# Performance work log

Hardware: AMD Instinct MI355X
Metric: run time of the kernel (lower is better)

Reference implementation:

```python
import jax, jax.numpy as jnp
import numpy as np

B, S, D, H = 4, 2048, 1024, 16
HD = D // H  # head_dim = 64


def setup_inputs() -> dict:
    key = jax.random.key(0)
    ks = jax.random.split(key, 11)
    scale = 1.0 / np.sqrt(D)
    q = jax.random.normal(ks[0], (B, S, D), jnp.float32)
    k = jax.random.normal(ks[1], (B, S, D), jnp.float32)
    v = jax.random.normal(ks[2], (B, S, D), jnp.float32)
    # causal mask, broadcastable over [B, H, Sq, Sk]
    mask = jnp.tril(jnp.ones((S, S), bool))[None, None, :, :]
    Wq = jax.random.normal(ks[3], (D, D), jnp.float32) * scale
    bq = jnp.zeros((D,), jnp.float32)
    Wk = jax.random.normal(ks[4], (D, D), jnp.float32) * scale
    bk = jnp.zeros((D,), jnp.float32)
    Wv = jax.random.normal(ks[5], (D, D), jnp.float32) * scale
    bv = jnp.zeros((D,), jnp.float32)
    Wo = jax.random.normal(ks[6], (D, D), jnp.float32) * scale
    bo = jnp.zeros((D,), jnp.float32)
    return {"q": q, "k": k, "v": v, "mask": mask,
            "Wq": Wq, "bq": bq, "Wk": Wk, "bk": bk,
            "Wv": Wv, "bv": bv, "Wo": Wo, "bo": bo}


def reference(q, k, v, mask, Wq, bq, Wk, bk, Wv, bv, Wo, bo):
    b, sq, _ = q.shape
    sk = k.shape[1]
    # projections (torch Linear: x @ W.T + b)
    qh = (q @ Wq.T + bq).reshape(b, sq, H, HD)
    kh = (k @ Wk.T + bk).reshape(b, sk, H, HD)
    vh = (v @ Wv.T + bv).reshape(b, sk, H, HD)
    # scaled dot-product attention: [b, h, sq, sk]
    scores = jnp.einsum('bqhd,bkhd->bhqk', qh, kh) / jnp.sqrt(jnp.float32(HD))
    scores = jnp.where(mask, scores, jnp.float32(-jnp.inf))
    attn = jax.nn.softmax(scores, axis=-1)
    out = jnp.einsum('bhqk,bkhd->bqhd', attn, vh).reshape(b, sq, D)
    return out @ Wo.T + bo
```

## Files before the change

### kernel.cpp

```cpp
#include <hip/hip_runtime.h>
#include <hip/hip_bf16.h>
#include <cstdint>
#include <cstddef>

typedef __attribute__((ext_vector_type(4))) float f32x4;
typedef __attribute__((ext_vector_type(8))) __bf16 bf16x8;

constexpr int Bc = 4, Sc = 2048, Dc = 1024, Hc = 16, HDc = 64;
constexpr int Mrows = Bc * Sc;
constexpr int Kdim = Dc;

__device__ __forceinline__ void gload_lds16(const void* g, void* lds) {
  __builtin_amdgcn_global_load_lds(
      (const __attribute__((address_space(1))) void*)g,
      (__attribute__((address_space(3))) void*)lds, 16, 0, 0);
}

__global__ void cvt4_f32_to_bf16(const float* __restrict__ s0, const float* __restrict__ s1,
                                 const float* __restrict__ s2, const float* __restrict__ s3,
                                 __bf16* __restrict__ d0, __bf16* __restrict__ d1,
                                 __bf16* __restrict__ d2, __bf16* __restrict__ d3, int n4each) {
  int i = blockIdx.x * blockDim.x + threadIdx.x;
  int which = i / n4each, j = i - which * n4each;
  const float* s = which == 0 ? s0 : which == 1 ? s1 : which == 2 ? s2 : s3;
  __bf16* d = which == 0 ? d0 : which == 1 ? d1 : which == 2 ? d2 : d3;
  float4 f = ((const float4*)s)[j];
  union { __bf16 h[4]; uint2 u; } p;
  p.h[0] = (__bf16)f.x; p.h[1] = (__bf16)f.y;
  p.h[2] = (__bf16)f.z; p.h[3] = (__bf16)f.w;
  ((uint2*)d)[j] = p.u;
}

__global__ __launch_bounds__(256, 2)
void gemm_qkv(const float* __restrict__ qin, const float* __restrict__ kin,
              const float* __restrict__ vin, const __bf16* __restrict__ Wcat,
              const float* __restrict__ bq, const float* __restrict__ bk,
              const float* __restrict__ bv,
              __bf16* __restrict__ Qh, __bf16* __restrict__ Kh,
              __bf16* __restrict__ Vt, float qscale)
{
  __shared__ __align__(16) __bf16 As[128 * 32];
  __shared__ __align__(16) __bf16 Bs[128 * 32];
  const int tid = threadIdx.x;
  const int wave = tid >> 6, lane = tid & 63;
  const int wr = wave >> 1, wc = wave & 1;
  const int r = lane & 15, hi = lane >> 4;
  const int lin = (int)blockIdx.y * 24 + (int)blockIdx.x;
  const int xcd = lin & 7, s8 = lin >> 3;
  const int my = (xcd << 3) | (s8 / 24);
  const int mx = s8 % 24;
  const int m0 = my * 128, n0 = mx * 128;
  const int proj = n0 >> 10;
  const float* Xa = proj == 0 ? qin : proj == 1 ? kin : vin;

  f32x4 acc[4][4] = {};

  for (int k0 = 0; k0 < Kdim; k0 += 32) {
    #pragma unroll
    for (int c = 0; c < 2; ++c) {
      int chunk = c * 256 + tid;
      int row = chunk >> 2;
      int cw = chunk & 3;
      int hc = cw ^ (row & 3);
      const float* src = Xa + (size_t)(m0 + row) * Kdim + k0 + hc * 8;
      float4 f0 = *(const float4*)src;
      float4 f1 = *(const float4*)(src + 4);
      union { __bf16 h[8]; uint4 u; } pk;
      pk.h[0] = (__bf16)f0.x; pk.h[1] = (__bf16)f0.y;
      pk.h[2] = (__bf16)f0.z; pk.h[3] = (__bf16)f0.w;
      pk.h[4] = (__bf16)f1.x; pk.h[5] = (__bf16)f1.y;
      pk.h[6] = (__bf16)f1.z; pk.h[7] = (__bf16)f1.w;
      *(uint4*)&As[(size_t)chunk * 8] = pk.u;
    }
    #pragma unroll
    for (int c = 0; c < 2; ++c) {
      int chunk = c * 256 + wave * 64 + lane;
      int row = chunk >> 2;
      int hc = (chunk & 3) ^ (row & 3);
      gload_lds16(Wcat + (size_t)(n0 + row) * Kdim + k0 + hc * 8,
                  &Bs[(size_t)(c * 256 + wave * 64) * 8]);
    }
    __syncthreads();
    bf16x8 af[4], bfr[4];
    #pragma unroll
    for (int m = 0; m < 4; ++m) {
      int rowl = wr * 64 + m * 16 + r;
      af[m] = *(const bf16x8*)&As[rowl * 32 + ((hi ^ (rowl & 3)) * 8)];
    }
    #pragma unroll
    for (int n = 0; n < 4; ++n) {
      int rowl = wc * 64 + n * 16 + r;
      bfr[n] = *(const bf16x8*)&Bs[rowl * 32 + ((hi ^ (rowl & 3)) * 8)];
    }
    #pragma unroll
    for (int m = 0; m < 4; ++m)
      #pragma unroll
      for (int n = 0; n < 4; ++n)
        acc[m][n] = __builtin_amdgcn_mfma_f32_16x16x32_bf16(af[m], bfr[n], acc[m][n], 0, 0, 0);
    __syncthreads();
  }

  const float* bias = proj == 0 ? bq : proj == 1 ? bk : bv;
  if (proj < 2) {
    __bf16* out = proj == 0 ? Qh : Kh;
    const float sc = proj == 0 ? qscale : 1.0f;
    #pragma unroll
    for (int m = 0; m < 4; ++m)
      #pragma unroll
      for (int n = 0; n < 4; ++n)
        #pragma unroll
        for (int rg = 0; rg < 4; ++rg) {
          int row_g = m0 + wr * 64 + m * 16 + hi * 4 + rg;
          int col_g = n0 + wc * 64 + n * 16 + r;
          int c = col_g & 1023, h = c >> 6, d = c & 63;
          int b = row_g >> 11, s = row_g & (Sc - 1);
          float v = (acc[m][n][rg] + bias[c]) * sc;
          out[((((size_t)b * Hc + h) * Sc + s) << 6) + d] = (__bf16)v;
        }
  } else {
    #pragma unroll
    for (int m = 0; m < 4; ++m)
      #pragma unroll
      for (int n = 0; n < 4; ++n) {
        int row0 = m0 + wr * 64 + m * 16 + hi * 4;
        int col_g = n0 + wc * 64 + n * 16 + r;
        int c = col_g & 1023, h = c >> 6, d = c & 63;
        int b = row0 >> 11, s = row0 & (Sc - 1);
        union { __bf16 hh[4]; uint2 u; } w;
        #pragma unroll
        for (int rg = 0; rg < 4; ++rg)
          w.hh[rg] = (__bf16)(acc[m][n][rg] + bias[c]);
        *(uint2*)&Vt[((((size_t)b * Hc + h) * HDc + d) << 11) + s] = w.u;
      }
  }
}

__global__ __launch_bounds__(256, 2)
void gemm_out(const __bf16* __restrict__ A, const __bf16* __restrict__ Bw,
              const float* __restrict__ bias, float* __restrict__ outp)
{
  __shared__ __align__(16) __bf16 As[128 * 32];
  __shared__ __align__(16) __bf16 Bs[128 * 32];
  const int tid = threadIdx.x;
  const int wave = tid >> 6, lane = tid & 63;
  const int wr = wave >> 1, wc = wave & 1;
  const int r = lane & 15, hi = lane >> 4;
  const int lin = (int)blockIdx.y * 8 + (int)blockIdx.x;
  const int xcd = lin & 7, s8 = lin >> 3;
  const int m0 = (((xcd << 3) | (s8 >> 3)) ) * 128;
  const int n0 = (s8 & 7) * 128;

  f32x4 acc[4][4] = {};

  for (int k0 = 0; k0 < Kdim; k0 += 32) {
    #pragma unroll
    for (int c = 0; c < 2; ++c) {
      int chunk = c * 256 + wave * 64 + lane;
      int row = chunk >> 2;
      int hc = (chunk & 3) ^ (row & 3);
      gload_lds16(A  + (size_t)(m0 + row) * Kdim + k0 + hc * 8,
                  &As[(size_t)(c * 256 + wave * 64) * 8]);
      gload_lds16(Bw + (size_t)(n0 + row) * Kdim + k0 + hc * 8,
                  &Bs[(size_t)(c * 256 + wave * 64) * 8]);
    }
    __syncthreads();
    bf16x8 af[4], bfr[4];
    #pragma unroll
    for (int m = 0; m < 4; ++m) {
      int rowl = wr * 64 + m * 16 + r;
      af[m] = *(const bf16x8*)&As[rowl * 32 + ((hi ^ (rowl & 3)) * 8)];
    }
    #pragma unroll
    for (int n = 0; n < 4; ++n) {
      int rowl = wc * 64 + n * 16 + r;
      bfr[n] = *(const bf16x8*)&Bs[rowl * 32 + ((hi ^ (rowl & 3)) * 8)];
    }
    #pragma unroll
    for (int m = 0; m < 4; ++m)
      #pragma unroll
      for (int n = 0; n < 4; ++n)
        acc[m][n] = __builtin_amdgcn_mfma_f32_16x16x32_bf16(af[m], bfr[n], acc[m][n], 0, 0, 0);
    __syncthreads();
  }

  #pragma unroll
  for (int m = 0; m < 4; ++m)
    #pragma unroll
    for (int n = 0; n < 4; ++n)
      #pragma unroll
      for (int rg = 0; rg < 4; ++rg) {
        int row_g = m0 + wr * 64 + m * 16 + hi * 4 + rg;
        int col_g = n0 + wc * 64 + n * 16 + r;
        outp[(size_t)row_g * Dc + col_g] = acc[m][n][rg] + bias[col_g];
      }
}

__global__ __launch_bounds__(128, 2)
void attn_causal(const __bf16* __restrict__ Qh, const __bf16* __restrict__ Kh,
                 const __bf16* __restrict__ Vt, __bf16* __restrict__ outp)
{
  __shared__ __align__(16) float OaS[4][4][64][4];
  __shared__ float MS[4][64];
  __shared__ float LS[4][64];

  const int tid = threadIdx.x;
  const int wave = tid >> 6, lane = tid & 63;
  const int r = lane & 15, hi = lane >> 4;
  const int lin = (int)blockIdx.y * 32 + (int)blockIdx.x;
  const int xcd = lin & 7, s8 = lin >> 3;
  const int bh = (xcd << 3) | (s8 >> 5);
  const int qt = 31 - (s8 & 31);
  const int q0 = qt * 64;
  const __bf16* Q = Qh + (size_t)bh * (Sc * HDc);
  const __bf16* K = Kh + (size_t)bh * (Sc * HDc);
  const __bf16* V = Vt + (size_t)bh * (HDc * Sc);

  bf16x8 qf[4][2];
  #pragma unroll
  for (int m = 0; m < 4; ++m)
    #pragma unroll
    for (int kc = 0; kc < 2; ++kc)
      qf[m][kc] = *(const bf16x8*)&Q[(size_t)(q0 + m * 16 + r) * 64 + kc * 32 + hi * 8];

  f32x4 o_acc[4][4] = {};
  float mrow[4], lrow[4];
  #pragma unroll
  for (int m = 0; m < 4; ++m) { mrow[m] = -1e30f; lrow[m] = 0.f; }

  const int T = qt + 1;
  const int half = (T + 1) >> 1;
  const int t0 = wave ? half : 0;
  const int t1 = wave ? T : half;

  bf16x8 kf[4][2], vf[4][2], pb[4][2];

  #pragma unroll
  for (int n = 0; n < 4; ++n)
    #pragma unroll
    for (int kc = 0; kc < 2; ++kc) {
      kf[n][kc] = *(const bf16x8*)&K[(size_t)(t0 * 64 + n * 16 + r) * 64 + kc * 32 + hi * 8];
      vf[n][kc] = *(const bf16x8*)&V[(size_t)(n * 16 + r) * Sc + t0 * 64 + kc * 32 + hi * 8];
    }

  for (int t = t0; t < t1; ++t) {
    const bool diag = (t == T - 1);
    const int kvn = (t + 1) * 64;

    #pragma unroll
    for (int m = 0; m < 4; ++m) {
      f32x4 sn[4];
      __builtin_amdgcn_s_setprio(1);
      #pragma unroll
      for (int n = 0; n < 4; ++n) {
        f32x4 z = {0.f, 0.f, 0.f, 0.f};
        sn[n] = __builtin_amdgcn_mfma_f32_16x16x32_bf16(kf[n][0], qf[m][0], z, 0, 0, 0);
        sn[n] = __builtin_amdgcn_mfma_f32_16x16x32_bf16(kf[n][1], qf[m][1], sn[n], 0, 0, 0);
      }
      __builtin_amdgcn_s_setprio(0);
      if (diag) {
        #pragma unroll
        for (int n = 0; n < 4; ++n)
          #pragma unroll
          for (int rg = 0; rg < 4; ++rg)
            if (n * 16 + hi * 4 + rg > m * 16 + r) sn[n][rg] = -1e30f;
      }
      float mx = fmaxf(fmaxf(fmaxf(sn[0][0], sn[0][1]), fmaxf(sn[0][2], sn[0][3])),
                       fmaxf(fmaxf(sn[1][0], sn[1][1]), fmaxf(sn[1][2], sn[1][3])));
      mx = fmaxf(mx, fmaxf(fmaxf(fmaxf(sn[2][0], sn[2][1]), fmaxf(sn[2][2], sn[2][3])),
                           fmaxf(fmaxf(sn[3][0], sn[3][1]), fmaxf(sn[3][2], sn[3][3]))));
      mx = fmaxf(mx, __shfl_xor(mx, 16));
      mx = fmaxf(mx, __shfl_xor(mx, 32));
      float mloc = mrow[m];
      if (__any(mx > mloc + 8.f)) {
        float mnew = fmaxf(mloc, mx);
        float sc = __builtin_exp2f(mloc - mnew);
        lrow[m] *= sc;
        #pragma unroll
        for (int n = 0; n < 4; ++n) o_acc[m][n] *= sc;
        mrow[m] = mnew; mloc = mnew;
      }
      float rs = 0.f;
      #pragma unroll
      for (int n = 0; n < 4; ++n)
        #pragma unroll
        for (int rg = 0; rg < 4; ++rg) {
          float p = __builtin_exp2f(sn[n][rg] - mloc);
          sn[n][rg] = p;
          rs += p;
        }
      rs += __shfl_xor(rs, 16);
      rs += __shfl_xor(rs, 32);
      lrow[m] += rs;

      #pragma unroll
      for (int kc = 0; kc < 2; ++kc) {
        uint32_t p0a, p0b, p1a, p1b;
        asm("v_cvt_pk_bf16_f32 %0, %1, %2" : "=v"(p0a) : "v"(sn[2*kc][0]),   "v"(sn[2*kc][1]));
        asm("v_cvt_pk_bf16_f32 %0, %1, %2" : "=v"(p0b) : "v"(sn[2*kc][2]),   "v"(sn[2*kc][3]));
        asm("v_cvt_pk_bf16_f32 %0, %1, %2" : "=v"(p1a) : "v"(sn[2*kc+1][0]), "v"(sn[2*kc+1][1]));
        asm("v_cvt_pk_bf16_f32 %0, %1, %2" : "=v"(p1b) : "v"(sn[2*kc+1][2]), "v"(sn[2*kc+1][3]));
        asm("v_permlane32_swap_b32 %0, %1" : "+v"(p0a), "+v"(p1a));
        asm("v_permlane32_swap_b32 %0, %1" : "+v"(p0b), "+v"(p1b));
        uint32_t Xa = (uint32_t)__shfl_xor((int)p1a, 16);
        uint32_t Xb = (uint32_t)__shfl_xor((int)p1b, 16);
        uint32_t Ya = (uint32_t)__shfl_xor((int)p0a, 16);
        uint32_t Yb = (uint32_t)__shfl_xor((int)p0b, 16);
        union { uint32_t u[4]; bf16x8 v; } pk;
        pk.u[0] = (hi & 1) ? Xa : p0a;
        pk.u[1] = (hi & 1) ? Xb : p0b;
        pk.u[2] = (hi & 1) ? p1a : Ya;
        pk.u[3] = (hi & 1) ? p1b : Yb;
        pb[m][kc] = pk.v;
      }
    }

    if (t + 1 < t1) {
      #pragma unroll
      for (int n = 0; n < 4; ++n)
        #pragma unroll
        for (int kc = 0; kc < 2; ++kc)
          kf[n][kc] = *(const bf16x8*)&K[(size_t)(kvn + n * 16 + r) * 64 + kc * 32 + hi * 8];
    }

    __builtin_amdgcn_s_setprio(1);
    #pragma unroll
    for (int m = 0; m < 4; ++m)
      #pragma unroll
      for (int n = 0; n < 4; ++n) {
        o_acc[m][n] = __builtin_amdgcn_mfma_f32_16x16x32_bf16(vf[n][0], pb[m][0], o_acc[m][n], 0, 0, 0);
        o_acc[m][n] = __builtin_amdgcn_mfma_f32_16x16x32_bf16(vf[n][1], pb[m][1], o_acc[m][n], 0, 0, 0);
      }
    __builtin_amdgcn_s_setprio(0);

    if (t + 1 < t1) {
      #pragma unroll
      for (int n = 0; n < 4; ++n)
        #pragma unroll
        for (int kc = 0; kc < 2; ++kc)
          vf[n][kc] = *(const bf16x8*)&V[(size_t)(n * 16 + r) * Sc + kvn + kc * 32 + hi * 8];
    }
  }

  if (wave == 1) {
    #pragma unroll
    for (int m = 0; m < 4; ++m) {
      MS[m][lane] = mrow[m];
      LS[m][lane] = lrow[m];
      #pragma unroll
      for (int n = 0; n < 4; ++n)
        *(f32x4*)OaS[m][n][lane] = o_acc[m][n];
    }
  }
  __syncthreads();
  if (wave == 0) {
    const int b = bh >> 4, h = bh & 15;
    #pragma unroll
    for (int m = 0; m < 4; ++m) {
      float mB = MS[m][lane], lB = LS[m][lane];
      float mF = fmaxf(mrow[m], mB);
      float aA = __builtin_exp2f(mrow[m] - mF);
      float aB = __builtin_exp2f(mB - mF);
      float inv = 1.f / (lrow[m] * aA + lB * aB);
      size_t row = (size_t)b * Sc + q0 + m * 16 + r;
      #pragma unroll
      for (int n = 0; n < 4; ++n) {
        f32x4 oB = *(f32x4*)OaS[m][n][lane];
        union { __bf16 hh[4]; uint2 u; } w;
        #pragma unroll
        for (int rg = 0; rg < 4; ++rg)
          w.hh[rg] = (__bf16)((o_acc[m][n][rg] * aA + oB[rg] * aB) * inv);
        int col = h * 64 + n * 16 + hi * 4;
        *(uint2*)&outp[row * Dc + col] = w.u;
      }
    }
  }
}

extern "C" void kernel_launch(void* const* d_in, const int* in_sizes, int n_in,
                              void* d_out, int out_size, void* d_ws, size_t ws_size,
                              hipStream_t stream) {
  const float* q  = (const float*)d_in[0];
  const float* k  = (const float*)d_in[1];
  const float* v  = (const float*)d_in[2];
  const float* Wq = (const float*)d_in[4];
  const float* bq = (const float*)d_in[5];
  const float* Wk = (const float*)d_in[6];
  const float* bk = (const float*)d_in[7];
  const float* Wv = (const float*)d_in[8];
  const float* bv = (const float*)d_in[9];
  const float* Wo = (const float*)d_in[10];
  const float* bo = (const float*)d_in[11];

  char* ws = (char*)d_ws;
  constexpr size_t MB = 1u << 20;
  __bf16* Wcat = (__bf16*)(ws + 0 * MB);
  __bf16* Wkb  = (__bf16*)(ws + 2 * MB);
  __bf16* Wvb  = (__bf16*)(ws + 4 * MB);
  __bf16* Wob  = (__bf16*)(ws + 6 * MB);
  __bf16* Xbf  = (__bf16*)(ws + 8 * MB);
  __bf16* QhB  = (__bf16*)(ws + 24 * MB);
  __bf16* KhB  = (__bf16*)(ws + 40 * MB);
  __bf16* VtB  = (__bf16*)(ws + 56 * MB);

  const int nW4 = (Dc * Dc) / 4;
  cvt4_f32_to_bf16<<<(4 * nW4) / 256, 256, 0, stream>>>(Wq, Wk, Wv, Wo, Wcat, Wkb, Wvb, Wob, nW4);

  const float qscale = 0.125f * 1.44269504f;
  gemm_qkv<<<dim3(24, Mrows / 128), 256, 0, stream>>>(q, k, v, Wcat, bq, bk, bv,
                                                      QhB, KhB, VtB, qscale);

  attn_causal<<<dim3(32, Bc * Hc), 128, 0, stream>>>(QhB, KhB, VtB, Xbf);

  gemm_out<<<dim3(8, Mrows / 128), 256, 0, stream>>>(Xbf, Wob, bo, (float*)d_out);
}
```

Before: 279.3 us.

## Split causal attention work by paired 32-row query tiles instead of KV halves

Each wave now owns an independent 32-row query tile, pairing a short tile (px) with a long one (63-px) inside a block to balance causal work, instead of two waves splitting one 64-row tile's KV range. This removes the LDS merge of partial softmax states and the block barrier, and halves per-wave accumulator registers. In exchange each wave reloads the full K/V stream for only 32 query rows, so K/V reuse per load is halved, and the diagonal tile still computes a full 64-key block with masking.

```diff
diff --git a/kernel.cpp b/kernel.cpp
--- a/kernel.cpp
+++ b/kernel.cpp
@@ -199,55 +199,50 @@
 void attn_causal(const __bf16* __restrict__ Qh, const __bf16* __restrict__ Kh,
                  const __bf16* __restrict__ Vt, __bf16* __restrict__ outp)
 {
-  __shared__ __align__(16) float OaS[4][4][64][4];
-  __shared__ float MS[4][64];
-  __shared__ float LS[4][64];
-
   const int tid = threadIdx.x;
   const int wave = tid >> 6, lane = tid & 63;
   const int r = lane & 15, hi = lane >> 4;
   const int lin = (int)blockIdx.y * 32 + (int)blockIdx.x;
   const int xcd = lin & 7, s8 = lin >> 3;
   const int bh = (xcd << 3) | (s8 >> 5);
-  const int qt = 31 - (s8 & 31);
-  const int q0 = qt * 64;
+  const int px = s8 & 31;
+  const int qh = wave ? (63 - px) : px;
+  const int q0 = qh * 32;
   const __bf16* Q = Qh + (size_t)bh * (Sc * HDc);
   const __bf16* K = Kh + (size_t)bh * (Sc * HDc);
   const __bf16* V = Vt + (size_t)bh * (HDc * Sc);
 
-  bf16x8 qf[4][2];
-  #pragma unroll
-  for (int m = 0; m < 4; ++m)
+  bf16x8 qf[2][2];
+  #pragma unroll
+  for (int m = 0; m < 2; ++m)
     #pragma unroll
     for (int kc = 0; kc < 2; ++kc)
       qf[m][kc] = *(const bf16x8*)&Q[(size_t)(q0 + m * 16 + r) * 64 + kc * 32 + hi * 8];
 
-  f32x4 o_acc[4][4] = {};
-  float mrow[4], lrow[4];
-  #pragma unroll
-  for (int m = 0; m < 4; ++m) { mrow[m] = -1e30f; lrow[m] = 0.f; }
-
-  const int T = qt + 1;
-  const int half = (T + 1) >> 1;
-  const int t0 = wave ? half : 0;
-  const int t1 = wave ? T : half;
-
-  bf16x8 kf[4][2], vf[4][2], pb[4][2];
+  f32x4 o_acc[2][4] = {};
+  float mrow[2], lrow[2];
+  #pragma unroll
+  for (int m = 0; m < 2; ++m) { mrow[m] = -1e30f; lrow[m] = 0.f; }
+
+  const int T = (qh >> 1) + 1;
+  const int qloc_base = (qh & 1) * 32;
+
+  bf16x8 kf[4][2], vf[4][2], pb[2][2];
 
   #pragma unroll
   for (int n = 0; n < 4; ++n)
     #pragma unroll
     for (int kc = 0; kc < 2; ++kc) {
-      kf[n][kc] = *(const bf16x8*)&K[(size_t)(t0 * 64 + n * 16 + r) * 64 + kc * 32 + hi * 8];
-      vf[n][kc] = *(const bf16x8*)&V[(size_t)(n * 16 + r) * Sc + t0 * 64 + kc * 32 + hi * 8];
-    }
-
-  for (int t = t0; t < t1; ++t) {
+      kf[n][kc] = *(const bf16x8*)&K[(size_t)(n * 16 + r) * 64 + kc * 32 + hi * 8];
+      vf[n][kc] = *(const bf16x8*)&V[(size_t)(n * 16 + r) * Sc + kc * 32 + hi * 8];
+    }
+
+  for (int t = 0; t < T; ++t) {
     const bool diag = (t == T - 1);
     const int kvn = (t + 1) * 64;
 
     #pragma unroll
-    for (int m = 0; m < 4; ++m) {
+    for (int m = 0; m < 2; ++m) {
       f32x4 sn[4];
       __builtin_amdgcn_s_setprio(1);
       #pragma unroll
@@ -262,7 +257,7 @@
         for (int n = 0; n < 4; ++n)
           #pragma unroll
           for (int rg = 0; rg < 4; ++rg)
-            if (n * 16 + hi * 4 + rg > m * 16 + r) sn[n][rg] = -1e30f;
+            if (n * 16 + hi * 4 + rg > qloc_base + m * 16 + r) sn[n][rg] = -1e30f;
       }
       float mx = fmaxf(fmaxf(fmaxf(sn[0][0], sn[0][1]), fmaxf(sn[0][2], sn[0][3])),
                        fmaxf(fmaxf(sn[1][0], sn[1][1]), fmaxf(sn[1][2], sn[1][3])));
@@ -314,7 +309,7 @@
       }
     }
 
-    if (t + 1 < t1) {
+    if (t + 1 < T) {
       #pragma unroll
       for (int n = 0; n < 4; ++n)
         #pragma unroll
@@ -324,7 +319,7 @@
 
     __builtin_amdgcn_s_setprio(1);
     #pragma unroll
-    for (int m = 0; m < 4; ++m)
+    for (int m = 0; m < 2; ++m)
       #pragma unroll
       for (int n = 0; n < 4; ++n) {
         o_acc[m][n] = __builtin_amdgcn_mfma_f32_16x16x32_bf16(vf[n][0], pb[m][0], o_acc[m][n], 0, 0, 0);
@@ -332,7 +327,7 @@
       }
     __builtin_amdgcn_s_setprio(0);
 
-    if (t + 1 < t1) {
+    if (t + 1 < T) {
       #pragma unroll
       for (int n = 0; n < 4; ++n)
         #pragma unroll
@@ -341,37 +336,19 @@
     }
   }
 
-  if (wave == 1) {
-    #pragma unroll
-    for (int m = 0; m < 4; ++m) {
-      MS[m][lane] = mrow[m];
-      LS[m][lane] = lrow[m];
-      #pragma unroll
-      for (int n = 0; n < 4; ++n)
-        *(f32x4*)OaS[m][n][lane] = o_acc[m][n];
-    }
-  }
-  __syncthreads();
-  if (wave == 0) {
-    const int b = bh >> 4, h = bh & 15;
-    #pragma unroll
-    for (int m = 0; m < 4; ++m) {
-      float mB = MS[m][lane], lB = LS[m][lane];
-      float mF = fmaxf(mrow[m], mB);
-      float aA = __builtin_exp2f(mrow[m] - mF);
-      float aB = __builtin_exp2f(mB - mF);
-      float inv = 1.f / (lrow[m] * aA + lB * aB);
-      size_t row = (size_t)b * Sc + q0 + m * 16 + r;
-      #pragma unroll
-      for (int n = 0; n < 4; ++n) {
-        f32x4 oB = *(f32x4*)OaS[m][n][lane];
-        union { __bf16 hh[4]; uint2 u; } w;
-        #pragma unroll
-        for (int rg = 0; rg < 4; ++rg)
-          w.hh[rg] = (__bf16)((o_acc[m][n][rg] * aA + oB[rg] * aB) * inv);
-        int col = h * 64 + n * 16 + hi * 4;
-        *(uint2*)&outp[row * Dc + col] = w.u;
-      }
+  const int b = bh >> 4, h = bh & 15;
+  #pragma unroll
+  for (int m = 0; m < 2; ++m) {
+    float inv = 1.f / lrow[m];
+    size_t row = (size_t)b * Sc + q0 + m * 16 + r;
+    #pragma unroll
+    for (int n = 0; n < 4; ++n) {
+      union { __bf16 hh[4]; uint2 u; } w;
+      #pragma unroll
+      for (int rg = 0; rg < 4; ++rg)
+        w.hh[rg] = (__bf16)(o_acc[m][n][rg] * inv);
+      int col = h * 64 + n * 16 + hi * 4;
+      *(uint2*)&outp[row * Dc + col] = w.u;
     }
   }
 }
```

New measurement: 267.1 us. -4.4%, faster.
